# Performance work log

Hardware: AMD Instinct MI355X
Metric: run time of the kernel (lower is better)

## Reference

```python
import jax, jax.numpy as jnp
import numpy as np

DIM = 512
NL = 4
P = 8
B = 4
L = 8192  # byte-level sequence length
LP = L // P  # patch-level sequence length


def _ln(x, g, b, eps=1e-5):
    m = jnp.mean(x, axis=-1, keepdims=True)
    v = jnp.mean((x - m) ** 2, axis=-1, keepdims=True)
    return (x - m) * jax.lax.rsqrt(v + eps) * g + b


def setup_inputs() -> dict:
    key = jax.random.key(0)
    ks = jax.random.split(key, 24)
    s = 0.02
    inp = {
        "bytes_in": jax.random.randint(ks[0], (B, L), 0, 256, dtype=jnp.int32),
        "byte_emb": jax.random.normal(ks[1], (256, DIM), jnp.float32) * s,
        # patch encoder Conv1d(kernel=stride=P): weight laid out [P, D_in, D_out]
        "enc_w": jax.random.normal(ks[2], (P, DIM, DIM), jnp.float32) * s,
        "enc_b": jnp.zeros((DIM,), jnp.float32),
        "hash_proj": jax.random.normal(ks[3], (DIM, DIM), jnp.float32) * s,
        # per-layer stacked params
        "qkv_w": jax.random.normal(ks[4], (NL, DIM, 3 * DIM), jnp.float32) * s,
        "qkv_b": jnp.zeros((NL, 3 * DIM), jnp.float32),
        "gate_w": jax.random.normal(ks[5], (NL, DIM, DIM), jnp.float32) * s,
        "gate_b": jnp.zeros((NL, DIM), jnp.float32),
        "ln1_g": jnp.ones((NL, DIM), jnp.float32),
        "ln1_b": jnp.zeros((NL, DIM), jnp.float32),
        "mlp_w1": jax.random.normal(ks[6], (NL, DIM, 4 * DIM), jnp.float32) * s,
        "mlp_b1": jnp.zeros((NL, 4 * DIM), jnp.float32),
        "mlp_w2": jax.random.normal(ks[7], (NL, 4 * DIM, DIM), jnp.float32) * s,
        "mlp_b2": jnp.zeros((NL, DIM), jnp.float32),
        "ln2_g": jnp.ones((NL, DIM), jnp.float32),
        "ln2_b": jnp.zeros((NL, DIM), jnp.float32),
        # patch decoder ConvTranspose1d(kernel=stride=P): weight [D_in, P, D_out]
        "dec_w": jax.random.normal(ks[8], (DIM, P, DIM), jnp.float32) * s,
        "dec_b": jnp.zeros((DIM,), jnp.float32),
        "head_w": jax.random.normal(ks[9], (DIM, 256), jnp.float32) * s,
        "head_b": jnp.zeros((256,), jnp.float32),
    }
    return inp


def reference(bytes_in, byte_emb, enc_w, enc_b, hash_proj,
              qkv_w, qkv_b, gate_w, gate_b, ln1_g, ln1_b,
              mlp_w1, mlp_b1, mlp_w2, mlp_b2, ln2_g, ln2_b,
              dec_w, dec_b, head_w, head_b):
    # byte embedding: [B, L, D]
    x = byte_emb[bytes_in]
    # non-overlapping Conv1d(kernel=stride=P) == patch-wise contraction
    xp = x.reshape(B, LP, P, DIM)
    x = jnp.einsum('blpd,pdo->blo', xp, enc_w) + enc_b  # [B, LP, D]
    # hash projection
    x = x + jnp.tanh(x @ hash_proj)
    for i in range(NL):
        # LinearLatentKernel
        h = _ln(x, ln1_g[i], ln1_b[i])
        qkv = h @ qkv_w[i] + qkv_b[i]
        q, k, v = jnp.split(qkv, 3, axis=-1)
        kv_state = jnp.cumsum(k * v, axis=1)
        g = jax.nn.sigmoid(h @ gate_w[i] + gate_b[i])
        x = x + q * kv_state * g
        # MLP
        h = _ln(x, ln2_g[i], ln2_b[i])
        h = jax.nn.gelu(h @ mlp_w1[i] + mlp_b1[i], approximate=False)
        x = x + h @ mlp_w2[i] + mlp_b2[i]
    # ConvTranspose1d(kernel=stride=P): each patch expands to P positions
    y = jnp.einsum('bld,dpo->blpo', x, dec_w).reshape(B, L, DIM) + dec_b
    logits = y @ head_w + head_b  # [B, L, 256]
    return logits
```

## Files before the change

### kernel.cpp

```cpp
#include <hip/hip_runtime.h>
#include <hip/hip_bf16.h>
#include <math.h>

#define DIMD 512
#define NLAYER 4
#define PP 8
#define BBATCH 4
#define LBYTES 8192
#define LPATCH 1024
#define MROWS (BBATCH * LPATCH)

#define NCHUNK 64
#define CLEN   16
#define QGS    (4 * DIMD)

typedef __bf16 bf16x8 __attribute__((ext_vector_type(8)));
typedef float f32x4 __attribute__((ext_vector_type(4)));
typedef unsigned short u16x4 __attribute__((ext_vector_type(4)));
typedef unsigned short u16x8 __attribute__((ext_vector_type(8)));

__device__ __forceinline__ unsigned short f2bf(float f) {
    union { float f; unsigned u; } v; v.f = f;
    unsigned r = v.u + 0x7FFFu + ((v.u >> 16) & 1u);
    return (unsigned short)(r >> 16);
}
__device__ __forceinline__ float bf2f(unsigned short u) {
    union { unsigned u; float f; } v; v.u = ((unsigned)u) << 16;
    return v.f;
}

__device__ __forceinline__ void glds16(const unsigned short* g, unsigned short* l) {
    __builtin_amdgcn_global_load_lds((__attribute__((address_space(1))) void*)g,
                                     (__attribute__((address_space(3))) void*)l,
                                     16, 0, 0);
}

template<int TM, int ACT, bool BIAS, bool RES, bool OBF>
__global__ __launch_bounds__(256)
void mfma_gemm(const unsigned short* __restrict__ A, int lda, long aZ,
               const unsigned short* __restrict__ Bt, int ldb, long bZ,
               const float* __restrict__ bias,
               const float* __restrict__ res, int ldr,
               void* __restrict__ Cv, int ldc, long cZ, int K)
{
    constexpr int M_REP = TM / 32;
    __shared__ unsigned short As[TM * 32];
    __shared__ unsigned short Bs[128 * 32];

    const int tid = threadIdx.x;
    const int w = tid >> 6, l = tid & 63;
    const int row0 = blockIdx.x * TM;
    const int col0 = blockIdx.y * 128;
    A  += (size_t)blockIdx.z * aZ;
    Bt += (size_t)blockIdx.z * bZ;
    unsigned short* Cb = (unsigned short*)Cv + (size_t)blockIdx.z * cZ;
    float*          Cf = (float*)Cv          + (size_t)blockIdx.z * cZ;

    const int cA = w * 64 + l;
    const unsigned short* gA0 = A + (size_t)(row0 + (cA >> 2)) * lda + (cA & 3) * 8;
    const unsigned short* gB0 = Bt + (size_t)(col0 + (cA >> 2)) * ldb + (cA & 3) * 8;
    const unsigned short* gB1 = Bt + (size_t)(col0 + 64 + (cA >> 2)) * ldb + (cA & 3) * 8;
    unsigned short* lA0 = &As[w * 512];
    unsigned short* lB0 = &Bs[w * 512];
    unsigned short* lB1 = &Bs[2048 + w * 512];
    const unsigned short* gA1 = nullptr;
    unsigned short* lA1 = nullptr;
    if constexpr (TM == 128) {
        gA1 = A + (size_t)(row0 + 64 + (cA >> 2)) * lda + (cA & 3) * 8;
        lA1 = &As[2048 + w * 512];
    }

    const int wr = (w >> 1) * (TM / 2);
    const int wc = (w & 1) * 64;
    const int lr = l & 15, lk = (l >> 4) * 8;
    const int aBase = (wr + lr) * 32 + lk;
    const int bBase = (wc + lr) * 32 + lk;

    f32x4 acc[M_REP][4] = {};

    for (int k0 = 0; k0 < K; k0 += 32) {
        glds16(gA0, lA0);  gA0 += 32;
        if constexpr (TM == 128) { glds16(gA1, lA1); gA1 += 32; }
        glds16(gB0, lB0);  gB0 += 32;
        glds16(gB1, lB1);  gB1 += 32;
        __syncthreads();
        bf16x8 af[M_REP], bfr[4];
        #pragma unroll
        for (int m = 0; m < M_REP; m++)
            af[m] = *reinterpret_cast<const bf16x8*>(&As[aBase + m * 512]);
        #pragma unroll
        for (int n = 0; n < 4; n++)
            bfr[n] = *reinterpret_cast<const bf16x8*>(&Bs[bBase + n * 512]);
        #pragma unroll
        for (int m = 0; m < M_REP; m++)
            #pragma unroll
            for (int n = 0; n < 4; n++)
                acc[m][n] = __builtin_amdgcn_mfma_f32_16x16x32_bf16(
                    af[m], bfr[n], acc[m][n], 0, 0, 0);
        __syncthreads();
    }

    const int r0 = row0 + wr + (l >> 4) * 4;
    const int c0 = col0 + wc + lr;
    float bv[4] = {0.f, 0.f, 0.f, 0.f};
    if (BIAS) {
        #pragma unroll
        for (int n = 0; n < 4; n++) bv[n] = bias[c0 + n * 16];
    }
    #pragma unroll
    for (int m = 0; m < M_REP; m++) {
        #pragma unroll
        for (int j = 0; j < 4; j++) {
            const int row = r0 + m * 16 + j;
            #pragma unroll
            for (int n = 0; n < 4; n++) {
                float v = acc[m][n][j];
                if (BIAS) v += bv[n];
                if (ACT == 1) v = tanhf(v);
                if (ACT == 2) v = 0.5f * v * (1.f + erff(v * 0.70710678118f));
                if (RES) v += res[(size_t)row * ldr + c0 + n * 16];
                if (OBF) Cb[(size_t)row * ldc + c0 + n * 16] = f2bf(v);
                else     Cf[(size_t)row * ldc + c0 + n * 16] = v;
            }
        }
    }
}

__device__ __forceinline__ void packT64(float* sm, const float* __restrict__ in,
                                        unsigned short* __restrict__ out,
                                        int K, int N, int bk, int bn)
{
    float (*t)[65] = (float(*)[65])sm;
    const int k0 = bk * 64, n0 = bn * 64;
    const int tx = threadIdx.x & 63, ty = threadIdx.x >> 6;
    #pragma unroll
    for (int i = 0; i < 16; i++)
        t[ty + i * 4][tx] = in[(size_t)(k0 + ty + i * 4) * N + n0 + tx];
    __syncthreads();
    #pragma unroll
    for (int i = 0; i < 16; i++)
        out[(size_t)(n0 + ty + i * 4) * K + k0 + tx] = f2bf(t[tx][ty + i * 4]);
}

__device__ __forceinline__ void cast_body(const float* __restrict__ in,
                                          unsigned short* __restrict__ out, int blk)
{
    const long i = ((long)blk * 256 + threadIdx.x) * 8;
    float4 a = *(const float4*)(in + i);
    float4 b = *(const float4*)(in + i + 4);
    u16x8 o;
    o[0] = f2bf(a.x); o[1] = f2bf(a.y); o[2] = f2bf(a.z); o[3] = f2bf(a.w);
    o[4] = f2bf(b.x); o[5] = f2bf(b.y); o[6] = f2bf(b.z); o[7] = f2bf(b.w);
    *reinterpret_cast<u16x8*>(out + i) = o;
}

__global__ __launch_bounds__(256)
void megapack(const float* __restrict__ qkv_w, const float* __restrict__ gate_w,
              const float* __restrict__ mlp_w1, const float* __restrict__ mlp_w2,
              const float* __restrict__ hash_proj, const float* __restrict__ head_w,
              const float* __restrict__ enc_w, const float* __restrict__ dec_w,
              const float* __restrict__ byte_emb,
              const float* __restrict__ qkv_b, const float* __restrict__ gate_b,
              const float* __restrict__ dec_b, const float* __restrict__ head_b,
              unsigned short* __restrict__ wcat, unsigned short* __restrict__ w1T,
              unsigned short* __restrict__ w2T, unsigned short* __restrict__ whashT,
              unsigned short* __restrict__ hwT, unsigned short* __restrict__ encT,
              unsigned short* __restrict__ decb, unsigned short* __restrict__ embB,
              float* __restrict__ cbias, float* __restrict__ fb)
{
    __shared__ float sm[64 * 65];
    int id = blockIdx.x;
    if (id < 768) {
        int z = id / 192, r = id % 192;
        packT64(sm, qkv_w + (size_t)z * 512 * 1536, wcat + (size_t)z * 2048 * 512,
                512, 1536, r % 8, r / 8);
    } else if (id < 1024) {
        id -= 768; int z = id / 64, r = id % 64;
        packT64(sm, gate_w + (size_t)z * 512 * 512,
                wcat + (size_t)z * 2048 * 512 + (size_t)1536 * 512,
                512, 512, r % 8, r / 8);
    } else if (id < 2048) {
        id -= 1024; int z = id / 256, r = id % 256;
        packT64(sm, mlp_w1 + (size_t)z * 512 * 2048, w1T + (size_t)z * 2048 * 512,
                512, 2048, r % 8, r / 8);
    } else if (id < 3072) {
        id -= 2048; int z = id / 256, r = id % 256;
        packT64(sm, mlp_w2 + (size_t)z * 2048 * 512, w2T + (size_t)z * 512 * 2048,
                2048, 512, r & 31, r >> 5);
    } else if (id < 3136) {
        id -= 3072;
        packT64(sm, hash_proj, whashT, 512, 512, id % 8, id / 8);
    } else if (id < 3168) {
        id -= 3136;
        packT64(sm, head_w, hwT, 512, 256, id % 8, id / 8);
    } else if (id < 3680) {
        id -= 3168; int z = id / 64, r = id % 64;
        packT64(sm, enc_w + (size_t)z * 512 * 512, encT + (size_t)z * 512 * 512,
                512, 512, r % 8, r / 8);
    } else if (id < 4704) {
        cast_body(dec_w, decb, id - 3680);
    } else if (id < 4768) {
        cast_body(byte_emb, embB, id - 4704);
    } else if (id < 4800) {
        id -= 4768;
        const int i = id >> 3;
        const int n = (id & 7) * 256 + threadIdx.x;
        cbias[i * 2048 + n] = (n < 1536) ? qkv_b[i * 1536 + n] : gate_b[i * 512 + n - 1536];
    } else {
        const int o = threadIdx.x;
        float s = head_b[o];
        for (int d = 0; d < DIMD; d++) s = fmaf(dec_b[d], head_w[d * 256 + o], s);
        #pragma unroll
        for (int p = 0; p < PP; p++) fb[p * 256 + o] = s;
    }
}

__global__ __launch_bounds__(256)
void ln_kernel(const float* __restrict__ x, const float* __restrict__ g,
               const float* __restrict__ b, unsigned short* __restrict__ h)
{
    const int row = blockIdx.x * 4 + (threadIdx.x >> 6);
    const int lane = threadIdx.x & 63;
    const float* xr = x + (long)row * DIMD;
    float4 v0 = *(const float4*)(xr + lane * 8);
    float4 v1 = *(const float4*)(xr + lane * 8 + 4);
    float xv[8] = {v0.x, v0.y, v0.z, v0.w, v1.x, v1.y, v1.z, v1.w};
    float s = 0.f, q = 0.f;
    #pragma unroll
    for (int j = 0; j < 8; j++) { s += xv[j]; q += xv[j] * xv[j]; }
    #pragma unroll
    for (int off = 1; off < 64; off <<= 1) {
        s += __shfl_xor(s, off);
        q += __shfl_xor(q, off);
    }
    const float mean = s * (1.f / DIMD);
    const float var  = q * (1.f / DIMD) - mean * mean;
    const float rstd = rsqrtf(var + 1e-5f);
    float4 g0 = *(const float4*)(g + lane * 8);
    float4 g1 = *(const float4*)(g + lane * 8 + 4);
    float4 b0 = *(const float4*)(b + lane * 8);
    float4 b1 = *(const float4*)(b + lane * 8 + 4);
    float gv[8] = {g0.x, g0.y, g0.z, g0.w, g1.x, g1.y, g1.z, g1.w};
    float bb[8] = {b0.x, b0.y, b0.z, b0.w, b1.x, b1.y, b1.z, b1.w};
    u16x8 o;
    #pragma unroll
    for (int j = 0; j < 8; j++) o[j] = f2bf((xv[j] - mean) * rstd * gv[j] + bb[j]);
    *reinterpret_cast<u16x8*>(h + (long)row * DIMD + lane * 8) = o;
}

__global__ __launch_bounds__(128)
void embed_kernel(const int* __restrict__ bytes, const float* __restrict__ E,
                  const float* __restrict__ enc_b, float* __restrict__ x0,
                  unsigned short* __restrict__ x0b)
{
    const int patch = blockIdx.x;
    __shared__ int by[PP];
    if (threadIdx.x < PP) by[threadIdx.x] = bytes[patch * PP + threadIdx.x];
    __syncthreads();
    const int o = threadIdx.x * 4;
    float4 acc = *(const float4*)(enc_b + o);
    #pragma unroll
    for (int p = 0; p < PP; p++) {
        float4 e = *(const float4*)(E + ((long)(p * 256 + by[p])) * DIMD + o);
        acc.x += e.x; acc.y += e.y; acc.z += e.z; acc.w += e.w;
    }
    *(float4*)(x0 + (long)patch * DIMD + o) = acc;
    u16x4 ob; ob[0] = f2bf(acc.x); ob[1] = f2bf(acc.y);
    ob[2] = f2bf(acc.z); ob[3] = f2bf(acc.w);
    *reinterpret_cast<u16x4*>(x0b + (long)patch * DIMD + o) = ob;
}

__global__ __launch_bounds__(256)
void scan_partial(const unsigned short* __restrict__ qg, float* __restrict__ S)
{
    const int b = blockIdx.x >> 6, c = blockIdx.x & 63, d2 = threadIdx.x * 2;
    const unsigned short* base = qg + (size_t)(b * LPATCH + c * CLEN) * QGS;
    float s0 = 0.f, s1 = 0.f;
    for (int l = 0; l < CLEN; l++) {
        ushort2 kk = *(const ushort2*)(base + l * QGS + DIMD + d2);
        ushort2 vv = *(const ushort2*)(base + l * QGS + 2 * DIMD + d2);
        s0 = fmaf(bf2f(kk.x), bf2f(vv.x), s0);
        s1 = fmaf(bf2f(kk.y), bf2f(vv.y), s1);
    }
    *(float2*)(S + (size_t)(b * NCHUNK + c) * DIMD + d2) = make_float2(s0, s1);
}

__global__ __launch_bounds__(512)
void scan_prefix(float* __restrict__ S)
{
    const int b = blockIdx.x, d = threadIdx.x;
    float run = 0.f;
    #pragma unroll 4
    for (int c = 0; c < NCHUNK; c++) {
        float v = S[(b * NCHUNK + c) * DIMD + d];
        S[(b * NCHUNK + c) * DIMD + d] = run;
        run += v;
    }
}

__global__ __launch_bounds__(256)
void scan_apply(const unsigned short* __restrict__ qg,
                const float* __restrict__ S, float* __restrict__ x)
{
    const int b = blockIdx.x >> 6, c = blockIdx.x & 63, d2 = threadIdx.x * 2;
    float2 kv = *(const float2*)(S + (size_t)(b * NCHUNK + c) * DIMD + d2);
    const int row0 = b * LPATCH + c * CLEN;
    for (int l = 0; l < CLEN; l++) {
        const unsigned short* qb = qg + (size_t)(row0 + l) * QGS;
        ushort2 qq = *(const ushort2*)(qb + d2);
        ushort2 kk = *(const ushort2*)(qb + DIMD + d2);
        ushort2 vv = *(const ushort2*)(qb + 2 * DIMD + d2);
        ushort2 gg = *(const ushort2*)(qb + 3 * DIMD + d2);
        kv.x = fmaf(bf2f(kk.x), bf2f(vv.x), kv.x);
        kv.y = fmaf(bf2f(kk.y), bf2f(vv.y), kv.y);
        const float sg0 = 1.f / (1.f + expf(-bf2f(gg.x)));
        const float sg1 = 1.f / (1.f + expf(-bf2f(gg.y)));
        float* xr = x + (size_t)(row0 + l) * DIMD;
        float2 xv = *(const float2*)(xr + d2);
        xv.x += bf2f(qq.x) * kv.x * sg0;
        xv.y += bf2f(qq.y) * kv.y * sg1;
        *(float2*)(xr + d2) = xv;
    }
}

extern "C" void kernel_launch(void* const* d_in, const int* in_sizes, int n_in,
                              void* d_out, int out_size, void* d_ws, size_t ws_size,
                              hipStream_t stream)
{
    (void)in_sizes; (void)n_in; (void)out_size; (void)ws_size;

    const int*   bytes_in  = (const int*)d_in[0];
    const float* byte_emb  = (const float*)d_in[1];
    const float* enc_w     = (const float*)d_in[2];
    const float* enc_b     = (const float*)d_in[3];
    const float* hash_proj = (const float*)d_in[4];
    const float* qkv_w     = (const float*)d_in[5];
    const float* qkv_b     = (const float*)d_in[6];
    const float* gate_w    = (const float*)d_in[7];
    const float* gate_b    = (const float*)d_in[8];
    const float* ln1_g     = (const float*)d_in[9];
    const float* ln1_b     = (const float*)d_in[10];
    const float* mlp_w1    = (const float*)d_in[11];
    const float* mlp_b1    = (const float*)d_in[12];
    const float* mlp_w2    = (const float*)d_in[13];
    const float* mlp_b2    = (const float*)d_in[14];
    const float* ln2_g     = (const float*)d_in[15];
    const float* ln2_b     = (const float*)d_in[16];
    const float* dec_w     = (const float*)d_in[17];
    const float* dec_b     = (const float*)d_in[18];
    const float* head_w    = (const float*)d_in[19];
    const float* head_b    = (const float*)d_in[20];
    float* out = (float*)d_out;

    char* ws = (char*)d_ws;
    size_t o = 0;
    auto alloc = [&](size_t bytes) { char* p = ws + o; o += (bytes + 255) & ~(size_t)255; return p; };
    unsigned short* wcat   = (unsigned short*)alloc((size_t)4 * 2048 * 512 * 2);
    unsigned short* w1T    = (unsigned short*)alloc((size_t)4 * 2048 * 512 * 2);
    unsigned short* w2T    = (unsigned short*)alloc((size_t)4 * 512 * 2048 * 2);
    unsigned short* whashT = (unsigned short*)alloc((size_t)512 * 512 * 2);
    unsigned short* wWfT   = (unsigned short*)alloc((size_t)2048 * 512 * 2);
    unsigned short* encT   = (unsigned short*)alloc((size_t)8 * 512 * 512 * 2);
    unsigned short* hwT    = (unsigned short*)alloc((size_t)256 * 512 * 2);
    unsigned short* decb   = (unsigned short*)alloc((size_t)512 * 8 * 512 * 2);
    unsigned short* embB   = (unsigned short*)alloc((size_t)256 * 512 * 2);
    float* cbias           = (float*)alloc((size_t)4 * 2048 * 4);
    float* fb              = (float*)alloc(2048 * 4);
    float* E               = (float*)alloc((size_t)8 * 256 * 512 * 4);
    float* x               = (float*)alloc((size_t)MROWS * DIMD * 4);
    float* x0              = (float*)alloc((size_t)MROWS * DIMD * 4);
    unsigned short* x0b    = (unsigned short*)alloc((size_t)MROWS * DIMD * 2);
    unsigned short* h      = (unsigned short*)alloc((size_t)MROWS * DIMD * 2);
    unsigned short* xb     = (unsigned short*)alloc((size_t)MROWS * DIMD * 2);
    float* S               = (float*)alloc((size_t)BBATCH * NCHUNK * DIMD * 4);
    unsigned short* qg     = (unsigned short*)alloc((size_t)MROWS * 2048 * 2);
    unsigned short* hid    = (unsigned short*)alloc((size_t)MROWS * 2048 * 2);

    megapack<<<dim3(4801), 256, 0, stream>>>(
        qkv_w, gate_w, mlp_w1, mlp_w2, hash_proj, head_w, enc_w, dec_w, byte_emb,
        qkv_b, gate_b, dec_b, head_b,
        wcat, w1T, w2T, whashT, hwT, encT, decb, embB, cbias, fb);

    mfma_gemm<64, 0, false, false, true><<<dim3(4, 4, 8), 256, 0, stream>>>(
        hwT, 512, 0L, decb, PP * 512, 512L,
        nullptr, nullptr, 0, wWfT, 512, (long)256 * 512, 512);

    mfma_gemm<64, 0, false, false, false><<<dim3(4, 4, 8), 256, 0, stream>>>(
        embB, 512, 0L, encT, 512, (long)512 * 512,
        nullptr, nullptr, 0, E, 512, (long)256 * 512, 512);

    embed_kernel<<<dim3(MROWS), dim3(128), 0, stream>>>(bytes_in, E, enc_b, x0, x0b);

    mfma_gemm<64, 1, false, true, false><<<dim3(MROWS / 64, 4, 1), 256, 0, stream>>>(
        x0b, DIMD, 0L, whashT, DIMD, 0L, nullptr, x0, DIMD, x, DIMD, 0L, DIMD);

    for (int i = 0; i < NLAYER; i++) {
        ln_kernel<<<dim3(MROWS / 4), 256, 0, stream>>>(x, ln1_g + i * DIMD, ln1_b + i * DIMD, h);
        mfma_gemm<128, 0, true, false, true><<<dim3(MROWS / 128, 16, 1), 256, 0, stream>>>(
            h, DIMD, 0L, wcat + (size_t)i * 2048 * 512, DIMD, 0L,
            cbias + (size_t)i * 2048, nullptr, 0, qg, 2048, 0L, DIMD);
        scan_partial<<<dim3(BBATCH * NCHUNK), 256, 0, stream>>>(qg, S);
        scan_prefix<<<dim3(BBATCH), dim3(512), 0, stream>>>(S);
        scan_apply<<<dim3(BBATCH * NCHUNK), 256, 0, stream>>>(qg, S, x);
        ln_kernel<<<dim3(MROWS / 4), 256, 0, stream>>>(x, ln2_g + i * DIMD, ln2_b + i * DIMD, h);
        mfma_gemm<128, 2, true, false, true><<<dim3(MROWS / 128, 16, 1), 256, 0, stream>>>(
            h, DIMD, 0L, w1T + (size_t)i * 2048 * 512, DIMD, 0L,
            mlp_b1 + (size_t)i * 2048, nullptr, 0, hid, 2048, 0L, DIMD);
        if (i < NLAYER - 1) {
            mfma_gemm<64, 0, true, true, false><<<dim3(MROWS / 64, 4, 1), 256, 0, stream>>>(
                hid, 2048, 0L, w2T + (size_t)i * 512 * 2048, 2048, 0L,
                mlp_b2 + (size_t)i * DIMD, x, DIMD, x, DIMD, 0L, 2048);
        } else {
            mfma_gemm<64, 0, true, true, true><<<dim3(MROWS / 64, 4, 1), 256, 0, stream>>>(
                hid, 2048, 0L, w2T + (size_t)i * 512 * 2048, 2048, 0L,
                mlp_b2 + (size_t)i * DIMD, x, DIMD, xb, DIMD, 0L, 2048);
        }
    }

    mfma_gemm<128, 0, true, false, false><<<dim3(MROWS / 128, 16, 1), 256, 0, stream>>>(
        xb, DIMD, 0L, wWfT, DIMD, 0L, fb, nullptr, 0, out, 2048, 0L, DIMD);
}
```

Before: 489.7 us.

## Fuse scan apply with second layernorm and vectorize weight transpose loads

Merges the chunk scan-apply step with the following layernorm into one kernel. Each of 8 wavefronts owns two rows of a 16-row chunk and recomputes the in-chunk k*v prefix up to its rows, then applies the gated update, writes x, and does a wave-level layernorm reduction to emit bf16 h. This removes a separate LN launch and one full read of x, at the cost of redundant prefix recomputation across waves. The weight-packing transpose also switches to float2 global loads with a padded shared tile.

New measurement: 485.3 us. About the same (-0.9%).

```diff
diff --git a/kernel.cpp b/kernel.cpp
--- a/kernel.cpp
+++ b/kernel.cpp
@@ -130,13 +130,17 @@
                                         unsigned short* __restrict__ out,
                                         int K, int N, int bk, int bn)
 {
-    float (*t)[65] = (float(*)[65])sm;
+    float (*t)[66] = (float(*)[66])sm;
     const int k0 = bk * 64, n0 = bn * 64;
+    const int r = threadIdx.x >> 5;
+    const int c2 = (threadIdx.x & 31) * 2;
+    #pragma unroll
+    for (int i = 0; i < 8; i++) {
+        float2 v = *(const float2*)(in + (size_t)(k0 + r + i * 8) * N + n0 + c2);
+        *(float2*)&t[r + i * 8][c2] = v;
+    }
+    __syncthreads();
     const int tx = threadIdx.x & 63, ty = threadIdx.x >> 6;
-    #pragma unroll
-    for (int i = 0; i < 16; i++)
-        t[ty + i * 4][tx] = in[(size_t)(k0 + ty + i * 4) * N + n0 + tx];
-    __syncthreads();
     #pragma unroll
     for (int i = 0; i < 16; i++)
         out[(size_t)(n0 + ty + i * 4) * K + k0 + tx] = f2bf(t[tx][ty + i * 4]);
@@ -168,7 +172,7 @@
               unsigned short* __restrict__ decb, unsigned short* __restrict__ embB,
               float* __restrict__ cbias, float* __restrict__ fb)
 {
-    __shared__ float sm[64 * 65];
+    __shared__ float sm[64 * 66];
     int id = blockIdx.x;
     if (id < 768) {
         int z = id / 192, r = id % 192;
@@ -298,28 +302,78 @@
     }
 }
 
-__global__ __launch_bounds__(256)
-void scan_apply(const unsigned short* __restrict__ qg,
-                const float* __restrict__ S, float* __restrict__ x)
-{
-    const int b = blockIdx.x >> 6, c = blockIdx.x & 63, d2 = threadIdx.x * 2;
-    float2 kv = *(const float2*)(S + (size_t)(b * NCHUNK + c) * DIMD + d2);
+__global__ __launch_bounds__(512)
+void scan_apply_ln(const unsigned short* __restrict__ qg,
+                   const float* __restrict__ S, float* __restrict__ x,
+                   const float* __restrict__ lg, const float* __restrict__ lb,
+                   unsigned short* __restrict__ h)
+{
+    const int b = blockIdx.x >> 6, c = blockIdx.x & 63;
+    const int w = threadIdx.x >> 6, lane = threadIdx.x & 63;
+    const int d0 = lane * 8;
+
+    float kv[8];
+    {
+        const float* Sp = S + (size_t)(b * NCHUNK + c) * DIMD + d0;
+        float4 a = *(const float4*)Sp;
+        float4 bq = *(const float4*)(Sp + 4);
+        kv[0] = a.x; kv[1] = a.y; kv[2] = a.z; kv[3] = a.w;
+        kv[4] = bq.x; kv[5] = bq.y; kv[6] = bq.z; kv[7] = bq.w;
+    }
     const int row0 = b * LPATCH + c * CLEN;
-    for (int l = 0; l < CLEN; l++) {
+    for (int l = 0; l < 2 * w; l++) {
         const unsigned short* qb = qg + (size_t)(row0 + l) * QGS;
-        ushort2 qq = *(const ushort2*)(qb + d2);
-        ushort2 kk = *(const ushort2*)(qb + DIMD + d2);
-        ushort2 vv = *(const ushort2*)(qb + 2 * DIMD + d2);
-        ushort2 gg = *(const ushort2*)(qb + 3 * DIMD + d2);
-        kv.x = fmaf(bf2f(kk.x), bf2f(vv.x), kv.x);
-        kv.y = fmaf(bf2f(kk.y), bf2f(vv.y), kv.y);
-        const float sg0 = 1.f / (1.f + expf(-bf2f(gg.x)));
-        const float sg1 = 1.f / (1.f + expf(-bf2f(gg.y)));
-        float* xr = x + (size_t)(row0 + l) * DIMD;
-        float2 xv = *(const float2*)(xr + d2);
-        xv.x += bf2f(qq.x) * kv.x * sg0;
-        xv.y += bf2f(qq.y) * kv.y * sg1;
-        *(float2*)(xr + d2) = xv;
+        u16x8 kk = *reinterpret_cast<const u16x8*>(qb + DIMD + d0);
+        u16x8 vv = *reinterpret_cast<const u16x8*>(qb + 2 * DIMD + d0);
+        #pragma unroll
+        for (int j = 0; j < 8; j++) kv[j] = fmaf(bf2f(kk[j]), bf2f(vv[j]), kv[j]);
+    }
+
+    float gv[8], bv[8];
+    {
+        float4 g0 = *(const float4*)(lg + d0);
+        float4 g1 = *(const float4*)(lg + d0 + 4);
+        float4 b0 = *(const float4*)(lb + d0);
+        float4 b1 = *(const float4*)(lb + d0 + 4);
+        gv[0] = g0.x; gv[1] = g0.y; gv[2] = g0.z; gv[3] = g0.w;
+        gv[4] = g1.x; gv[5] = g1.y; gv[6] = g1.z; gv[7] = g1.w;
+        bv[0] = b0.x; bv[1] = b0.y; bv[2] = b0.z; bv[3] = b0.w;
+        bv[4] = b1.x; bv[5] = b1.y; bv[6] = b1.z; bv[7] = b1.w;
+    }
+
+    for (int l = 2 * w; l < 2 * w + 2; l++) {
+        const unsigned short* qb = qg + (size_t)(row0 + l) * QGS;
+        u16x8 qq = *reinterpret_cast<const u16x8*>(qb + d0);
+        u16x8 kk = *reinterpret_cast<const u16x8*>(qb + DIMD + d0);
+        u16x8 vv = *reinterpret_cast<const u16x8*>(qb + 2 * DIMD + d0);
+        u16x8 gg = *reinterpret_cast<const u16x8*>(qb + 3 * DIMD + d0);
+        float* xr = x + (size_t)(row0 + l) * DIMD + d0;
+        float4 xv0 = *(const float4*)xr;
+        float4 xv1 = *(const float4*)(xr + 4);
+        float xold[8] = {xv0.x, xv0.y, xv0.z, xv0.w, xv1.x, xv1.y, xv1.z, xv1.w};
+        float xn[8];
+        float s = 0.f, qs = 0.f;
+        #pragma unroll
+        for (int j = 0; j < 8; j++) {
+            kv[j] = fmaf(bf2f(kk[j]), bf2f(vv[j]), kv[j]);
+            const float sg = 1.f / (1.f + expf(-bf2f(gg[j])));
+            const float nv = xold[j] + bf2f(qq[j]) * kv[j] * sg;
+            xn[j] = nv; s += nv; qs += nv * nv;
+        }
+        *(float4*)xr       = make_float4(xn[0], xn[1], xn[2], xn[3]);
+        *(float4*)(xr + 4) = make_float4(xn[4], xn[5], xn[6], xn[7]);
+        #pragma unroll
+        for (int off = 1; off < 64; off <<= 1) {
+            s += __shfl_xor(s, off);
+            qs += __shfl_xor(qs, off);
+        }
+        const float mean = s * (1.f / DIMD);
+        const float var  = qs * (1.f / DIMD) - mean * mean;
+        const float rstd = rsqrtf(var + 1e-5f);
+        u16x8 ho;
+        #pragma unroll
+        for (int j = 0; j < 8; j++) ho[j] = f2bf((xn[j] - mean) * rstd * gv[j] + bv[j]);
+        *reinterpret_cast<u16x8*>(h + (size_t)(row0 + l) * DIMD + d0) = ho;
     }
 }
 
@@ -401,8 +455,8 @@
             cbias + (size_t)i * 2048, nullptr, 0, qg, 2048, 0L, DIMD);
         scan_partial<<<dim3(BBATCH * NCHUNK), 256, 0, stream>>>(qg, S);
         scan_prefix<<<dim3(BBATCH), dim3(512), 0, stream>>>(S);
-        scan_apply<<<dim3(BBATCH * NCHUNK), 256, 0, stream>>>(qg, S, x);
-        ln_kernel<<<dim3(MROWS / 4), 256, 0, stream>>>(x, ln2_g + i * DIMD, ln2_b + i * DIMD, h);
+        scan_apply_ln<<<dim3(BBATCH * NCHUNK), dim3(512), 0, stream>>>(
+            qg, S, x, ln2_g + i * DIMD, ln2_b + i * DIMD, h);
         mfma_gemm<128, 2, true, false, true><<<dim3(MROWS / 128, 16, 1), 256, 0, stream>>>(
             h, DIMD, 0L, w1T + (size_t)i * 2048 * 512, DIMD, 0L,
             mlp_b1 + (size_t)i * 2048, nullptr, 0, hid, 2048, 0L, DIMD);
```
